# Kernel tuning notes

Hardware: AMD Instinct MI355X
Metric: run time of the kernel (lower is better)

Reference implementation:

```python
import jax, jax.numpy as jnp
import numpy as np

D_MODEL = 1024
NUM_HEADS = 16
D_K = D_MODEL // NUM_HEADS
B, S = 2, 2048


def setup_inputs() -> dict:
    key = jax.random.key(0)
    ks = jax.random.split(key, 4)
    scale = 1.0 / np.sqrt(D_MODEL)
    x = jax.random.normal(ks[0], (B, S, D_MODEL), dtype=jnp.float32)
    w_qkv = jax.random.normal(ks[1], (D_MODEL, 3 * D_MODEL), dtype=jnp.float32) * scale
    b_qkv = jnp.zeros((3 * D_MODEL,), dtype=jnp.float32)
    w_out = jax.random.normal(ks[2], (D_MODEL, D_MODEL), dtype=jnp.float32) * scale
    b_out = jnp.zeros((D_MODEL,), dtype=jnp.float32)
    # causal mask: 1 where attention is allowed (j <= i), 0 elsewhere
    mask = jnp.tril(jnp.ones((S, S), dtype=jnp.int32))
    return {"x": x, "mask": mask, "w_qkv": w_qkv, "b_qkv": b_qkv,
            "w_out": w_out, "b_out": b_out}


def reference(x, mask, w_qkv, b_qkv, w_out, b_out):
    Bb, Ss, C = x.shape
    qkv = x @ w_qkv + b_qkv                      # [B,S,3C]
    q, k, v = jnp.split(qkv, 3, axis=-1)
    def split_heads(t):
        return t.reshape(Bb, Ss, NUM_HEADS, D_K).transpose(0, 2, 1, 3)  # [B,H,S,Dk]
    q, k, v = split_heads(q), split_heads(k), split_heads(v)
    scores = jnp.einsum('bhqd,bhkd->bhqk', q, k) / jnp.sqrt(jnp.float32(D_K))
    scores = jnp.where(mask == 0, -jnp.inf, scores)
    weights = jax.nn.softmax(scores, axis=-1)
    weights = jnp.nan_to_num(weights, nan=0.0)   # matches torch.nan_to_num
    attn = jnp.einsum('bhqk,bhkd->bhqd', weights, v)
    attn = attn.transpose(0, 2, 1, 3).reshape(Bb, Ss, C)
    return attn @ w_out + b_out
```

## Files before the change

kernel.cpp:

```cpp
#include <hip/hip_runtime.h>
#include <hip/hip_bf16.h>

#define D_MODEL 1024
#define NUM_HEADS 16
#define D_K 64
#define BATCH 2
#define SEQ 2048

typedef __attribute__((ext_vector_type(8))) short bf16x8;
typedef __attribute__((ext_vector_type(4))) float f32x4;

union P16 { int4 i4; ushort u[8]; };
union FU { float f; unsigned int u; };

__device__ __forceinline__ float bf2f(ushort u) {
    union { unsigned int i; float f; } c; c.i = ((unsigned int)u) << 16; return c.f;
}
__device__ __forceinline__ ushort f2bf(float f) {
    union { float f; unsigned int i; } c; c.f = f;
    unsigned int x = c.i;
    return (ushort)((x + 0x7fff + ((x >> 16) & 1)) >> 16);
}
__device__ __forceinline__ unsigned int cvt_pk_bf16(float lo, float hi) {
    unsigned int r;
    asm("v_cvt_pk_bf16_f32 %0, %1, %2" : "=v"(r) : "v"(lo), "v"(hi));
    return r;
}

__device__ __forceinline__ bool wave_detect_f32(const ushort* x) {
    ushort u = x[2 * (threadIdx.x & 63)];
    int e = (u >> 7) & 0xFF;
    unsigned long long bl = __ballot(e >= 100 && e <= 141);
    return __popcll(bl) < 32;
}

__global__ __launch_bounds__(256)
void prep_all(const ushort* __restrict__ x, const void* __restrict__ Wq,
              const void* __restrict__ Wo, ushort* __restrict__ xb,
              ushort* __restrict__ WqT, ushort* __restrict__ WoT,
              int* __restrict__ flag)
{
    const bool f32 = wave_detect_f32(x);
    const int bx = blockIdx.x, tx = threadIdx.x;
    if (bx == 0 && tx == 0) flag[0] = f32 ? 1 : 0;

    if (bx >= 1024) {
        if (!f32) return;
        int i = ((bx - 1024) * 256 + tx) * 8;
        const float* f = (const float*)x + i;
        float4 a = *(const float4*)f, b = *(const float4*)(f + 4);
        P16 r;
        r.u[0] = f2bf(a.x); r.u[1] = f2bf(a.y); r.u[2] = f2bf(a.z); r.u[3] = f2bf(a.w);
        r.u[4] = f2bf(b.x); r.u[5] = f2bf(b.y); r.u[6] = f2bf(b.z); r.u[7] = f2bf(b.w);
        *(int4*)(xb + i) = r.i4;
        return;
    }

    __shared__ ushort t[64][72];
    const int nb = bx & 63, kb = bx >> 6;
    const void* W; ushort* WT; int N, n0;
    if (nb < 48) { W = Wq; WT = WqT; N = 3 * D_MODEL; n0 = nb * 64; }
    else         { W = Wo; WT = WoT; N = D_MODEL;     n0 = (nb - 48) * 64; }
    const int k0 = kb * 64, K = D_MODEL;
    #pragma unroll
    for (int p = 0; p < 16; ++p) {
        int r = p * 4 + (tx >> 6), c = tx & 63;
        float v = f32 ? ((const float*)W)[(size_t)(k0 + r) * N + n0 + c]
                      : bf2f(((const ushort*)W)[(size_t)(k0 + r) * N + n0 + c]);
        t[r][c] = f2bf(v);
    }
    __syncthreads();
    #pragma unroll
    for (int p = 0; p < 16; ++p) {
        int nn = p * 4 + (tx >> 6), kk = tx & 63;
        WT[(size_t)(n0 + nn) * K + k0 + kk] = t[kk][nn];
    }
}

template<int MODE>
__global__ __launch_bounds__(256)
void gemm128(const void* __restrict__ Araw, const ushort* __restrict__ Aconv,
             const ushort* __restrict__ WT, const void* __restrict__ bias,
             void* __restrict__ out, int N, int K, const int* __restrict__ flag)
{
    __shared__ ushort As[2][128 * 32];
    __shared__ ushort Bs[2][128 * 32];

    const int f = *flag;
    const ushort* A = (MODE == 1) ? (f ? Aconv : (const ushort*)Araw) : Aconv;

    const int tid = threadIdx.x;
    const int w = tid >> 6, lane = tid & 63;
    const int ln = lane & 15, quad = lane >> 4;
    const int m0 = blockIdx.y * 128, n0 = blockIdx.x * 128;
    const int wm = (w >> 1) * 64, wn = (w & 1) * 64;

    const int s0 = w * 128 + lane, s1 = s0 + 64;
    const int ar0 = s0 >> 2, ak0 = ((s0 & 3) ^ ((ar0 >> 1) & 3)) * 8;
    const int ar1 = s1 >> 2, ak1 = ((s1 & 3) ^ ((ar1 >> 1) & 3)) * 8;
    const size_t aoff0 = (size_t)(m0 + ar0) * K + ak0;
    const size_t aoff1 = (size_t)(m0 + ar1) * K + ak1;
    const size_t boff0 = (size_t)(n0 + ar0) * K + ak0;
    const size_t boff1 = (size_t)(n0 + ar1) * K + ak1;

    const int physc = (quad ^ ((ln >> 1) & 3)) * 8;

    f32x4 acc[4][4] = {};

    const int nk = K >> 5;
    int4 a0 = *(const int4*)(A + aoff0);
    int4 a1 = *(const int4*)(A + aoff1);
    int4 b0 = *(const int4*)(WT + boff0);
    int4 b1 = *(const int4*)(WT + boff1);
    *(int4*)(As[0] + s0 * 8) = a0;
    *(int4*)(As[0] + s1 * 8) = a1;
    *(int4*)(Bs[0] + s0 * 8) = b0;
    *(int4*)(Bs[0] + s1 * 8) = b1;
    a0 = *(const int4*)(A + aoff0 + 32);
    a1 = *(const int4*)(A + aoff1 + 32);
    b0 = *(const int4*)(WT + boff0 + 32);
    b1 = *(const int4*)(WT + boff1 + 32);
    __syncthreads();

    for (int kt = 0; kt < nk; ++kt) {
        const int cur = kt & 1;
        if (kt + 1 < nk) {
            *(int4*)(As[1 - cur] + s0 * 8) = a0;
            *(int4*)(As[1 - cur] + s1 * 8) = a1;
            *(int4*)(Bs[1 - cur] + s0 * 8) = b0;
            *(int4*)(Bs[1 - cur] + s1 * 8) = b1;
        }
        if (kt + 2 < nk) {
            const int kc = (kt + 2) * 32;
            a0 = *(const int4*)(A + aoff0 + kc);
            a1 = *(const int4*)(A + aoff1 + kc);
            b0 = *(const int4*)(WT + boff0 + kc);
            b1 = *(const int4*)(WT + boff1 + kc);
        }

        bf16x8 af[4], bf[4];
        #pragma unroll
        for (int t = 0; t < 4; ++t) {
            af[t] = *(const bf16x8*)(As[cur] + (wm + t * 16 + ln) * 32 + physc);
            bf[t] = *(const bf16x8*)(Bs[cur] + (wn + t * 16 + ln) * 32 + physc);
        }
        #pragma unroll
        for (int mi = 0; mi < 4; ++mi)
            #pragma unroll
            for (int ni = 0; ni < 4; ++ni)
                acc[mi][ni] = __builtin_amdgcn_mfma_f32_16x16x32_bf16(
                    af[mi], bf[ni], acc[mi][ni], 0, 0, 0);
        __syncthreads();
    }

    #pragma unroll
    for (int mi = 0; mi < 4; ++mi) {
        #pragma unroll
        for (int ni = 0; ni < 4; ++ni) {
            int col = n0 + wn + ni * 16 + ln;
            float bb = f ? ((const float*)bias)[col] : bf2f(((const ushort*)bias)[col]);
            #pragma unroll
            for (int r = 0; r < 4; ++r) {
                int row = m0 + wm + mi * 16 + quad * 4 + r;
                float v = acc[mi][ni][r] + bb;
                if (MODE == 0 && f) ((float*)out)[(size_t)row * N + col] = v;
                else                ((ushort*)out)[(size_t)row * N + col] = f2bf(v);
            }
        }
    }
}

template<int MODE>
__global__ __launch_bounds__(256)
void gemm64(const void* __restrict__ Araw, const ushort* __restrict__ Aconv,
            const ushort* __restrict__ WT, const void* __restrict__ bias,
            void* __restrict__ out, int N, int K, const int* __restrict__ flag)
{
    __shared__ ushort As[2][64 * 32];
    __shared__ ushort Bs[2][128 * 32];

    const int f = *flag;
    const ushort* A = (MODE == 1) ? (f ? Aconv : (const ushort*)Araw) : Aconv;

    const int tid = threadIdx.x;
    const int w = tid >> 6, lane = tid & 63;
    const int ln = lane & 15, quad = lane >> 4;
    const int m0 = blockIdx.y * 64, n0 = blockIdx.x * 128;
    const int wn = w * 32;

    const int sa = tid;
    const int arow = sa >> 2, akc = ((sa & 3) ^ ((arow >> 1) & 3)) * 8;
    const size_t aoff = (size_t)(m0 + arow) * K + akc;
    const int sb0 = tid, sb1 = tid + 256;
    const int br0 = sb0 >> 2, bk0 = ((sb0 & 3) ^ ((br0 >> 1) & 3)) * 8;
    const int br1 = sb1 >> 2, bk1 = ((sb1 & 3) ^ ((br1 >> 1) & 3)) * 8;
    const size_t boff0 = (size_t)(n0 + br0) * K + bk0;
    const size_t boff1 = (size_t)(n0 + br1) * K + bk1;

    const int physc = (quad ^ ((ln >> 1) & 3)) * 8;

    f32x4 acc[4][2] = {};

    const int nk = K >> 5;
    int4 a0 = *(const int4*)(A + aoff);
    int4 b0 = *(const int4*)(WT + boff0);
    int4 b1 = *(const int4*)(WT + boff1);
    *(int4*)(As[0] + sa * 8)  = a0;
    *(int4*)(Bs[0] + sb0 * 8) = b0;
    *(int4*)(Bs[0] + sb1 * 8) = b1;
    a0 = *(const int4*)(A + aoff + 32);
    b0 = *(const int4*)(WT + boff0 + 32);
    b1 = *(const int4*)(WT + boff1 + 32);
    __syncthreads();

    for (int kt = 0; kt < nk; ++kt) {
        const int cur = kt & 1;
        if (kt + 1 < nk) {
            *(int4*)(As[1 - cur] + sa * 8)  = a0;
            *(int4*)(Bs[1 - cur] + sb0 * 8) = b0;
            *(int4*)(Bs[1 - cur] + sb1 * 8) = b1;
        }
        if (kt + 2 < nk) {
            const int kc = (kt + 2) * 32;
            a0 = *(const int4*)(A + aoff + kc);
            b0 = *(const int4*)(WT + boff0 + kc);
            b1 = *(const int4*)(WT + boff1 + kc);
        }

        bf16x8 af[4], bf[2];
        #pragma unroll
        for (int t = 0; t < 4; ++t)
            af[t] = *(const bf16x8*)(As[cur] + (t * 16 + ln) * 32 + physc);
        #pragma unroll
        for (int t = 0; t < 2; ++t)
            bf[t] = *(const bf16x8*)(Bs[cur] + (wn + t * 16 + ln) * 32 + physc);
        #pragma unroll
        for (int mi = 0; mi < 4; ++mi)
            #pragma unroll
            for (int ni = 0; ni < 2; ++ni)
                acc[mi][ni] = __builtin_amdgcn_mfma_f32_16x16x32_bf16(
                    af[mi], bf[ni], acc[mi][ni], 0, 0, 0);
        __syncthreads();
    }

    #pragma unroll
    for (int mi = 0; mi < 4; ++mi) {
        #pragma unroll
        for (int ni = 0; ni < 2; ++ni) {
            int col = n0 + wn + ni * 16 + ln;
            float bb = f ? ((const float*)bias)[col] : bf2f(((const ushort*)bias)[col]);
            #pragma unroll
            for (int r = 0; r < 4; ++r) {
                int row = m0 + mi * 16 + quad * 4 + r;
                float v = acc[mi][ni][r] + bb;
                if (MODE == 0 && f) ((float*)out)[(size_t)row * N + col] = v;
                else                ((ushort*)out)[(size_t)row * N + col] = f2bf(v);
            }
        }
    }
}

__global__ __launch_bounds__(256)
void flash_attn11(const ushort* __restrict__ qkv, ushort* __restrict__ attn)
{
    __shared__ ushort Ks[64][72];
    __shared__ ushort Vs[64][72];
    __shared__ ushort QPs[128][72];

    const int tid  = threadIdx.x;
    const int wave = tid >> 6, lane = tid & 63;
    const int ln   = lane & 15, quad = lane >> 4;
    const int pg   = wave >> 1, ww = wave & 1;
    const int bh   = blockIdx.x;
    const int ky   = blockIdx.y;
    const int k    = (ky < 8) ? ky : 23 - ky;
    const int xx   = 2 * k + pg;
    const int b    = bh >> 4, hh = bh & (NUM_HEADS - 1);
    const int W3   = 3 * D_MODEL;
    const size_t hbase = (size_t)b * SEQ * W3 + hh * D_K;

    const int q0A = 32 * (63 - xx), q0B = 32 * xx;
    const int ntA = 32 - k, ntB = k + 1;

    const int qrr = tid >> 1, qcol = (tid & 1) * 32;
    const int ksr = tid >> 2, ksc = (tid & 3) * 16;
    const int vp  = tid & 31, vg = (tid >> 5) * 8;

    const int vkey = 2 * vp;
    const int vcol = (vkey & 32) + ((vkey >> 2) & 3) * 8 + ((vkey >> 4) & 1) * 4 + (vkey & 3);

    {
        const int qpg = qrr >> 6, qmt = (qrr >> 5) & 1, ql = qrr & 31;
        const int qxx = 2 * k + qpg;
        const int grow = qmt ? (32 * qxx + ql) : (32 * (63 - qxx) + ql);
        const ushort* src = qkv + hbase + (size_t)grow * W3 + qcol;
        #pragma unroll
        for (int h = 0; h < 4; ++h) {
            P16 v; v.i4 = *(const int4*)(src + h * 8);
            #pragma unroll
            for (int e = 0; e < 8; ++e) v.u[e] = f2bf(bf2f(v.u[e]) * 0.18033688011f);
            *(int4*)(&QPs[qrr][qcol + h * 8]) = v.i4;
        }
    }
    __syncthreads();
    bf16x8 qf[2][2];
    #pragma unroll
    for (int mt = 0; mt < 2; ++mt)
        #pragma unroll
        for (int s = 0; s < 2; ++s)
            qf[mt][s] = *(const bf16x8*)(&QPs[pg * 64 + mt * 32 + ww * 16 + ln][s * 32 + quad * 8]);

    f32x4 acc_o[2][4] = {};
    f32x4 acc_l[2] = {};

    bf16x8 ones8;
    #pragma unroll
    for (int e = 0; e < 8; ++e) ones8[e] = (short)0x3F80;

    const ushort* Kbase = qkv + hbase + D_MODEL;
    const ushort* Vbase = qkv + hbase + 2 * D_MODEL;

    int4 kreg[2], vreg[2];
    {
        const ushort* ksrc = Kbase + (size_t)ksr * W3 + ksc;
        kreg[0] = *(const int4*)(ksrc);
        kreg[1] = *(const int4*)(ksrc + 8);
        vreg[0] = *(const int4*)(Vbase + (size_t)(2 * vp)     * W3 + vg);
        vreg[1] = *(const int4*)(Vbase + (size_t)(2 * vp + 1) * W3 + vg);
    }

    for (int jt = 0; jt < ntA; ++jt) {
        const int j0 = jt * 64;
        const bool doB = (jt < ntB);
        __syncthreads();

        *(int4*)(&Ks[ksr][ksc])     = kreg[0];
        *(int4*)(&Ks[ksr][ksc + 8]) = kreg[1];
        {
            P16 v0, v1; v0.i4 = vreg[0]; v1.i4 = vreg[1];
            #pragma unroll
            for (int e = 0; e < 8; ++e) {
                unsigned int pack = (unsigned int)v0.u[e] | ((unsigned int)v1.u[e] << 16);
                *(unsigned int*)(&Vs[vg + e][vcol]) = pack;
            }
        }
        __syncthreads();

        if (jt + 1 < ntA) {
            const int jn = j0 + 64;
            const ushort* ksrc = Kbase + (size_t)(jn + ksr) * W3 + ksc;
            kreg[0] = *(const int4*)(ksrc);
            kreg[1] = *(const int4*)(ksrc + 8);
            vreg[0] = *(const int4*)(Vbase + (size_t)(jn + 2 * vp)     * W3 + vg);
            vreg[1] = *(const int4*)(Vbase + (size_t)(jn + 2 * vp + 1) * W3 + vg);
        }

        f32x4 sa[2][4];
        #pragma unroll
        for (int t = 0; t < 4; ++t) {
            bf16x8 k0 = *(const bf16x8*)(&Ks[t * 16 + ln][quad * 8]);
            bf16x8 k1 = *(const bf16x8*)(&Ks[t * 16 + ln][32 + quad * 8]);
            {
                f32x4 z = {};
                z = __builtin_amdgcn_mfma_f32_16x16x32_bf16(k0, qf[0][0], z, 0, 0, 0);
                z = __builtin_amdgcn_mfma_f32_16x16x32_bf16(k1, qf[0][1], z, 0, 0, 0);
                sa[0][t] = z;
            }
            if (doB) {
                f32x4 z = {};
                z = __builtin_amdgcn_mfma_f32_16x16x32_bf16(k0, qf[1][0], z, 0, 0, 0);
                z = __builtin_amdgcn_mfma_f32_16x16x32_bf16(k1, qf[1][1], z, 0, 0, 0);
                sa[1][t] = z;
            }
        }

        if (jt == ntA - 1) {
            const int qrow = q0A + ww * 16 + ln;
            #pragma unroll
            for (int t = 0; t < 4; ++t)
                #pragma unroll
                for (int r = 0; r < 4; ++r)
                    if (j0 + t * 16 + quad * 4 + r > qrow) sa[0][t][r] = -1e30f;
        }
        if (doB && jt == ntB - 1) {
            const int qrow = q0B + ww * 16 + ln;
            #pragma unroll
            for (int t = 0; t < 4; ++t)
                #pragma unroll
                for (int r = 0; r < 4; ++r)
                    if (j0 + t * 16 + quad * 4 + r > qrow) sa[1][t][r] = -1e30f;
        }

        union PB { unsigned int w[4]; bf16x8 v; };
        PB pa[2][2];
        #pragma unroll
        for (int mt = 0; mt < 2; ++mt) {
            if (mt && !doB) break;
            #pragma unroll
            for (int s = 0; s < 2; ++s) {
                #pragma unroll
                for (int w = 0; w < 4; ++w) {
                    const int t = 2 * s + (w >> 1);
                    const int r0 = (w & 1) * 2;
                    float lo = exp2f(sa[mt][t][r0]);
                    float hi = exp2f(sa[mt][t][r0 + 1]);
                    pa[mt][s].w[w] = cvt_pk_bf16(lo, hi);
                }
            }
        }

        #pragma unroll
        for (int s = 0; s < 2; ++s) {
            #pragma unroll
            for (int t = 0; t < 4; ++t) {
                bf16x8 vf = *(const bf16x8*)(&Vs[t * 16 + ln][s * 32 + quad * 8]);
                acc_o[0][t] = __builtin_amdgcn_mfma_f32_16x16x32_bf16(pa[0][s].v, vf, acc_o[0][t], 0, 0, 0);
                if (doB)
                    acc_o[1][t] = __builtin_amdgcn_mfma_f32_16x16x32_bf16(pa[1][s].v, vf, acc_o[1][t], 0, 0, 0);
            }
            acc_l[0] = __builtin_amdgcn_mfma_f32_16x16x32_bf16(pa[0][s].v, ones8, acc_l[0], 0, 0, 0);
            if (doB)
                acc_l[1] = __builtin_amdgcn_mfma_f32_16x16x32_bf16(pa[1][s].v, ones8, acc_l[1], 0, 0, 0);
        }
    }

    #pragma unroll
    for (int mt = 0; mt < 2; ++mt) {
        const int q0 = mt ? q0B : q0A;
        #pragma unroll
        for (int r = 0; r < 4; ++r) {
            float inv = 1.0f / acc_l[mt][r];
            int i = q0 + ww * 16 + quad * 4 + r;
            size_t rowoff = ((size_t)(b * SEQ + i)) * D_MODEL + hh * D_K;
            #pragma unroll
            for (int t = 0; t < 4; ++t)
                attn[rowoff + t * 16 + ln] = f2bf(acc_o[mt][t][r] * inv);
        }
    }
}

extern "C" void kernel_launch(void* const* d_in, const int* in_sizes, int n_in,
                              void* d_out, int out_size, void* d_ws, size_t ws_size,
                              hipStream_t stream)
{
    const void* x     = d_in[0];
    const void* w_qkv = d_in[2];
    const void* b_qkv = d_in[3];
    const void* w_out = d_in[4];
    const void* b_out = d_in[5];

    char* ws = (char*)d_ws;
    int*    flag   = (int*)ws;                  size_t off = 256;
    ushort* WqkvT  = (ushort*)(ws + off);       off += (size_t)3 * D_MODEL * D_MODEL * 2;
    ushort* WoutT  = (ushort*)(ws + off);       off += (size_t)D_MODEL * D_MODEL * 2;
    ushort* qkv_ws = (ushort*)(ws + off);       off += (size_t)BATCH * SEQ * 3 * D_MODEL * 2;
    ushort* xb     = (ushort*)(ws + off);
    ushort* attn_ws = xb;

    const int M = BATCH * SEQ;

    prep_all<<<3072, 256, 0, stream>>>((const ushort*)x, w_qkv, w_out,
                                       xb, WqkvT, WoutT, flag);

    gemm128<1><<<dim3(3 * D_MODEL / 128, M / 128), 256, 0, stream>>>(
        x, xb, WqkvT, b_qkv, qkv_ws, 3 * D_MODEL, D_MODEL, flag);

    dim3 ga(BATCH * NUM_HEADS, 16);
    flash_attn11<<<ga, 256, 0, stream>>>(qkv_ws, attn_ws);

    gemm64<0><<<dim3(D_MODEL / 128, M / 64), 256, 0, stream>>>(
        attn_ws, attn_ws, WoutT, b_out, d_out, D_MODEL, D_MODEL, flag);
}
```

Baseline: 212.8 us.

## Process two K/V tiles per barrier pair in flash attention

Restructures the attention key loop to stage 128 keys (two 64-key K tiles and two V tiles) in LDS per iteration, so the two block barriers are paid once per two tiles instead of per tile. The Q staging buffer is aliased onto the enlarged K buffer, which keeps LDS usage roughly unchanged but needs an extra barrier after the Q fragments are read. Register prefetch now holds twice as many K/V vectors, which raises register pressure and may lower occupancy.

```diff
diff --git a/kernel.cpp b/kernel.cpp
--- a/kernel.cpp
+++ b/kernel.cpp
@@ -261,11 +261,10 @@
 }
 
 __global__ __launch_bounds__(256)
-void flash_attn11(const ushort* __restrict__ qkv, ushort* __restrict__ attn)
+void flash_attn12(const ushort* __restrict__ qkv, ushort* __restrict__ attn)
 {
-    __shared__ ushort Ks[64][72];
-    __shared__ ushort Vs[64][72];
-    __shared__ ushort QPs[128][72];
+    __shared__ ushort Ks[128][72];
+    __shared__ ushort Vs[2][64][72];
 
     const int tid  = threadIdx.x;
     const int wave = tid >> 6, lane = tid & 63;
@@ -281,6 +280,7 @@
 
     const int q0A = 32 * (63 - xx), q0B = 32 * xx;
     const int ntA = 32 - k, ntB = k + 1;
+    const int nIt = (ntA + 1) >> 1;
 
     const int qrr = tid >> 1, qcol = (tid & 1) * 32;
     const int ksr = tid >> 2, ksc = (tid & 3) * 16;
@@ -299,7 +299,7 @@
             P16 v; v.i4 = *(const int4*)(src + h * 8);
             #pragma unroll
             for (int e = 0; e < 8; ++e) v.u[e] = f2bf(bf2f(v.u[e]) * 0.18033688011f);
-            *(int4*)(&QPs[qrr][qcol + h * 8]) = v.i4;
+            *(int4*)(&Ks[qrr][qcol + h * 8]) = v.i4;
         }
     }
     __syncthreads();
@@ -308,7 +308,8 @@
     for (int mt = 0; mt < 2; ++mt)
         #pragma unroll
         for (int s = 0; s < 2; ++s)
-            qf[mt][s] = *(const bf16x8*)(&QPs[pg * 64 + mt * 32 + ww * 16 + ln][s * 32 + quad * 8]);
+            qf[mt][s] = *(const bf16x8*)(&Ks[pg * 64 + mt * 32 + ww * 16 + ln][s * 32 + quad * 8]);
+    __syncthreads();
 
     f32x4 acc_o[2][4] = {};
     f32x4 acc_l[2] = {};
@@ -320,20 +321,24 @@
     const ushort* Kbase = qkv + hbase + D_MODEL;
     const ushort* Vbase = qkv + hbase + 2 * D_MODEL;
 
-    int4 kreg[2], vreg[2];
-    {
-        const ushort* ksrc = Kbase + (size_t)ksr * W3 + ksc;
+    int4 kreg[4], vreg[4];
+
+    auto load_regs = [&](int pair) {
+        const int j0 = pair * 128;
+        const ushort* ksrc = Kbase + (size_t)(j0 + ksr) * W3 + ksc;
         kreg[0] = *(const int4*)(ksrc);
         kreg[1] = *(const int4*)(ksrc + 8);
-        vreg[0] = *(const int4*)(Vbase + (size_t)(2 * vp)     * W3 + vg);
-        vreg[1] = *(const int4*)(Vbase + (size_t)(2 * vp + 1) * W3 + vg);
-    }
-
-    for (int jt = 0; jt < ntA; ++jt) {
-        const int j0 = jt * 64;
-        const bool doB = (jt < ntB);
-        __syncthreads();
-
+        vreg[0] = *(const int4*)(Vbase + (size_t)(j0 + 2 * vp)     * W3 + vg);
+        vreg[1] = *(const int4*)(Vbase + (size_t)(j0 + 2 * vp + 1) * W3 + vg);
+        if (2 * pair + 1 < ntA) {
+            const ushort* ksrc2 = ksrc + (size_t)64 * W3;
+            kreg[2] = *(const int4*)(ksrc2);
+            kreg[3] = *(const int4*)(ksrc2 + 8);
+            vreg[2] = *(const int4*)(Vbase + (size_t)(j0 + 64 + 2 * vp)     * W3 + vg);
+            vreg[3] = *(const int4*)(Vbase + (size_t)(j0 + 64 + 2 * vp + 1) * W3 + vg);
+        }
+    };
+    auto write_lds = [&](int pair) {
         *(int4*)(&Ks[ksr][ksc])     = kreg[0];
         *(int4*)(&Ks[ksr][ksc + 8]) = kreg[1];
         {
@@ -341,87 +346,108 @@
             #pragma unroll
             for (int e = 0; e < 8; ++e) {
                 unsigned int pack = (unsigned int)v0.u[e] | ((unsigned int)v1.u[e] << 16);
-                *(unsigned int*)(&Vs[vg + e][vcol]) = pack;
-            }
-        }
-        __syncthreads();
-
-        if (jt + 1 < ntA) {
-            const int jn = j0 + 64;
-            const ushort* ksrc = Kbase + (size_t)(jn + ksr) * W3 + ksc;
-            kreg[0] = *(const int4*)(ksrc);
-            kreg[1] = *(const int4*)(ksrc + 8);
-            vreg[0] = *(const int4*)(Vbase + (size_t)(jn + 2 * vp)     * W3 + vg);
-            vreg[1] = *(const int4*)(Vbase + (size_t)(jn + 2 * vp + 1) * W3 + vg);
-        }
-
-        f32x4 sa[2][4];
-        #pragma unroll
-        for (int t = 0; t < 4; ++t) {
-            bf16x8 k0 = *(const bf16x8*)(&Ks[t * 16 + ln][quad * 8]);
-            bf16x8 k1 = *(const bf16x8*)(&Ks[t * 16 + ln][32 + quad * 8]);
-            {
-                f32x4 z = {};
-                z = __builtin_amdgcn_mfma_f32_16x16x32_bf16(k0, qf[0][0], z, 0, 0, 0);
-                z = __builtin_amdgcn_mfma_f32_16x16x32_bf16(k1, qf[0][1], z, 0, 0, 0);
-                sa[0][t] = z;
-            }
-            if (doB) {
-                f32x4 z = {};
-                z = __builtin_amdgcn_mfma_f32_16x16x32_bf16(k0, qf[1][0], z, 0, 0, 0);
-                z = __builtin_amdgcn_mfma_f32_16x16x32_bf16(k1, qf[1][1], z, 0, 0, 0);
-                sa[1][t] = z;
-            }
-        }
-
-        if (jt == ntA - 1) {
-            const int qrow = q0A + ww * 16 + ln;
-            #pragma unroll
-            for (int t = 0; t < 4; ++t)
+                *(unsigned int*)(&Vs[0][vg + e][vcol]) = pack;
+            }
+        }
+        if (2 * pair + 1 < ntA) {
+            *(int4*)(&Ks[64 + ksr][ksc])     = kreg[2];
+            *(int4*)(&Ks[64 + ksr][ksc + 8]) = kreg[3];
+            P16 v0, v1; v0.i4 = vreg[2]; v1.i4 = vreg[3];
+            #pragma unroll
+            for (int e = 0; e < 8; ++e) {
+                unsigned int pack = (unsigned int)v0.u[e] | ((unsigned int)v1.u[e] << 16);
+                *(unsigned int*)(&Vs[1][vg + e][vcol]) = pack;
+            }
+        }
+    };
+
+    load_regs(0);
+    write_lds(0);
+    load_regs(1);
+    __syncthreads();
+
+    for (int it = 0; it < nIt; ++it) {
+        #pragma unroll
+        for (int st = 0; st < 2; ++st) {
+            const int jt = 2 * it + st;
+            if (st && jt >= ntA) break;
+            const int j0 = jt * 64;
+            const bool doB = (jt < ntB);
+            const int kb0 = st * 64;
+
+            f32x4 sa[2][4];
+            #pragma unroll
+            for (int t = 0; t < 4; ++t) {
+                bf16x8 k0 = *(const bf16x8*)(&Ks[kb0 + t * 16 + ln][quad * 8]);
+                bf16x8 k1 = *(const bf16x8*)(&Ks[kb0 + t * 16 + ln][32 + quad * 8]);
+                {
+                    f32x4 z = {};
+                    z = __builtin_amdgcn_mfma_f32_16x16x32_bf16(k0, qf[0][0], z, 0, 0, 0);
+                    z = __builtin_amdgcn_mfma_f32_16x16x32_bf16(k1, qf[0][1], z, 0, 0, 0);
+                    sa[0][t] = z;
+                }
+                if (doB) {
+                    f32x4 z = {};
+                    z = __builtin_amdgcn_mfma_f32_16x16x32_bf16(k0, qf[1][0], z, 0, 0, 0);
+                    z = __builtin_amdgcn_mfma_f32_16x16x32_bf16(k1, qf[1][1], z, 0, 0, 0);
+                    sa[1][t] = z;
+                }
+            }
+
+            if (jt == ntA - 1) {
+                const int qrow = q0A + ww * 16 + ln;
                 #pragma unroll
-                for (int r = 0; r < 4; ++r)
-                    if (j0 + t * 16 + quad * 4 + r > qrow) sa[0][t][r] = -1e30f;
-        }
-        if (doB && jt == ntB - 1) {
-            const int qrow = q0B + ww * 16 + ln;
-            #pragma unroll
-            for (int t = 0; t < 4; ++t)
+                for (int t = 0; t < 4; ++t)
+                    #pragma unroll
+                    for (int r = 0; r < 4; ++r)
+                        if (j0 + t * 16 + quad * 4 + r > qrow) sa[0][t][r] = -1e30f;
+            }
+            if (doB && jt == ntB - 1) {
+                const int qrow = q0B + ww * 16 + ln;
                 #pragma unroll
-                for (int r = 0; r < 4; ++r)
-                    if (j0 + t * 16 + quad * 4 + r > qrow) sa[1][t][r] = -1e30f;
-        }
-
-        union PB { unsigned int w[4]; bf16x8 v; };
-        PB pa[2][2];
-        #pragma unroll
-        for (int mt = 0; mt < 2; ++mt) {
-            if (mt && !doB) break;
+                for (int t = 0; t < 4; ++t)
+                    #pragma unroll
+                    for (int r = 0; r < 4; ++r)
+                        if (j0 + t * 16 + quad * 4 + r > qrow) sa[1][t][r] = -1e30f;
+            }
+
+            union PB { unsigned int w[4]; bf16x8 v; };
+            PB pa[2][2];
+            #pragma unroll
+            for (int mt = 0; mt < 2; ++mt) {
+                if (mt && !doB) break;
+                #pragma unroll
+                for (int s = 0; s < 2; ++s) {
+                    #pragma unroll
+                    for (int w = 0; w < 4; ++w) {
+                        const int t = 2 * s + (w >> 1);
+                        const int r0 = (w & 1) * 2;
+                        float lo = exp2f(sa[mt][t][r0]);
+                        float hi = exp2f(sa[mt][t][r0 + 1]);
+                        pa[mt][s].w[w] = cvt_pk_bf16(lo, hi);
+                    }
+                }
+            }
+
             #pragma unroll
             for (int s = 0; s < 2; ++s) {
                 #pragma unroll
-                for (int w = 0; w < 4; ++w) {
-                    const int t = 2 * s + (w >> 1);
-                    const int r0 = (w & 1) * 2;
-                    float lo = exp2f(sa[mt][t][r0]);
-                    float hi = exp2f(sa[mt][t][r0 + 1]);
-                    pa[mt][s].w[w] = cvt_pk_bf16(lo, hi);
+                for (int t = 0; t < 4; ++t) {
+                    bf16x8 vf = *(const bf16x8*)(&Vs[st][t * 16 + ln][s * 32 + quad * 8]);
+                    acc_o[0][t] = __builtin_amdgcn_mfma_f32_16x16x32_bf16(pa[0][s].v, vf, acc_o[0][t], 0, 0, 0);
+                    if (doB)
+                        acc_o[1][t] = __builtin_amdgcn_mfma_f32_16x16x32_bf16(pa[1][s].v, vf, acc_o[1][t], 0, 0, 0);
                 }
-            }
-        }
-
-        #pragma unroll
-        for (int s = 0; s < 2; ++s) {
-            #pragma unroll
-            for (int t = 0; t < 4; ++t) {
-                bf16x8 vf = *(const bf16x8*)(&Vs[t * 16 + ln][s * 32 + quad * 8]);
-                acc_o[0][t] = __builtin_amdgcn_mfma_f32_16x16x32_bf16(pa[0][s].v, vf, acc_o[0][t], 0, 0, 0);
+                acc_l[0] = __builtin_amdgcn_mfma_f32_16x16x32_bf16(pa[0][s].v, ones8, acc_l[0], 0, 0, 0);
                 if (doB)
-                    acc_o[1][t] = __builtin_amdgcn_mfma_f32_16x16x32_bf16(pa[1][s].v, vf, acc_o[1][t], 0, 0, 0);
-            }
-            acc_l[0] = __builtin_amdgcn_mfma_f32_16x16x32_bf16(pa[0][s].v, ones8, acc_l[0], 0, 0, 0);
-            if (doB)
-                acc_l[1] = __builtin_amdgcn_mfma_f32_16x16x32_bf16(pa[1][s].v, ones8, acc_l[1], 0, 0, 0);
-        }
+                    acc_l[1] = __builtin_amdgcn_mfma_f32_16x16x32_bf16(pa[1][s].v, ones8, acc_l[1], 0, 0, 0);
+            }
+        }
+
+        __syncthreads();
+        if (it + 1 < nIt) write_lds(it + 1);
+        if (it + 2 < nIt) load_regs(it + 2);
+        __syncthreads();
     }
 
     #pragma unroll
@@ -466,7 +492,7 @@
         x, xb, WqkvT, b_qkv, qkv_ws, 3 * D_MODEL, D_MODEL, flag);
 
     dim3 ga(BATCH * NUM_HEADS, 16);
-    flash_attn11<<<ga, 256, 0, stream>>>(qkv_ws, attn_ws);
+    flash_attn12<<<ga, 256, 0, stream>>>(qkv_ws, attn_ws);
 
     gemm64<0><<<dim3(D_MODEL / 128, M / 64), 256, 0, stream>>>(
         attn_ws, attn_ws, WoutT, b_out, d_out, D_MODEL, D_MODEL, flag);
```

Result: no change. 214.1 us (+0.6%).
